# Kernel optimization log

Measured on AMD Instinct MI355X. Metric: run time of the kernel, lower is better.

The kernel has to match this reference:

```python
import jax, jax.numpy as jnp
import numpy as np

C = 2.3026  # Poincare ball curvature
EPS = 1e-15

def _hlinear(x, z, r, c):
    # hypll-style Poincare fully connected layer (HNN++, Shimizu et al.)
    # x: (B, fi) on ball, z: (fi, fo), r: (fo,)
    cs = jnp.sqrt(c)
    lam = 2.0 / (1.0 - c * jnp.sum(x * x, axis=-1, keepdims=True))  # conformal factor (B,1)
    zn = jnp.maximum(jnp.sqrt(jnp.sum(z * z, axis=0)), EPS)         # (fo,)
    tcr = 2.0 * cs * r                                              # (fo,)
    # signed hyperplane distances v_k
    d = (2.0 * zn / cs) * jnp.arcsinh(
        cs * lam * (x @ z) / zn * jnp.cosh(tcr) - (lam - 1.0) * jnp.sinh(tcr))
    w = jnp.sinh(cs * d) / cs
    # map back into the ball: ||out|| < 1/sqrt(c)
    return w / (1.0 + jnp.sqrt(1.0 + c * jnp.sum(w * w, axis=-1, keepdims=True)))

def _hrelu(x, c):
    # logmap at origin -> ReLU in tangent space -> expmap at origin
    cs = jnp.sqrt(c)
    n = jnp.maximum(jnp.sqrt(jnp.sum(x * x, axis=-1, keepdims=True)), EPS)
    v = jnp.arctanh(jnp.minimum(cs * n, 1.0 - 1e-7)) * x / (cs * n)
    v = jax.nn.relu(v)
    vn = jnp.maximum(jnp.sqrt(jnp.sum(v * v, axis=-1, keepdims=True)), EPS)
    return jnp.tanh(cs * vn) * v / (cs * vn)

def setup_inputs() -> dict:
    key = jax.random.key(0)
    ks = jax.random.split(key, 9)
    B, D = 65536, 768
    xs = 0.02 * jax.random.normal(ks[0], (B, D), dtype=jnp.float32)
    # repo preprocessing: lift to Lorentz (K=C) then Lorentz->Poincare
    x0 = jnp.sqrt(1.0 / C + jnp.sum(xs * xs, axis=-1, keepdims=True))
    x = xs / (x0 + 1.0)  # strictly inside ball of radius 1/sqrt(C)
    def mk(k, fi, fo):
        return (jax.random.normal(k, (fi, fo), dtype=jnp.float32) / np.float32(np.sqrt(fi)))
    return {
        "x": x,
        "z1": mk(ks[1], 768, 512), "b1": 0.01 * jax.random.normal(ks[2], (512,), dtype=jnp.float32),
        "z2": mk(ks[3], 512, 256), "b2": 0.01 * jax.random.normal(ks[4], (256,), dtype=jnp.float32),
        "z3": mk(ks[5], 256, 128), "b3": 0.01 * jax.random.normal(ks[6], (128,), dtype=jnp.float32),
        "z4": mk(ks[7], 128, 1),   "b4": 0.01 * jax.random.normal(ks[8], (1,), dtype=jnp.float32),
    }

def reference(x, z1, b1, z2, b2, z3, b3, z4, b4):
    h = _hrelu(_hlinear(x, z1, b1, C), C)
    h = _hrelu(_hlinear(h, z2, b2, C), C)
    h = _hrelu(_hlinear(h, z3, b3, C), C)
    return _hlinear(h, z4, b4, C)
```

## Files before the change

kernel.cpp:

```cpp
#include <hip/hip_runtime.h>

#define CURV 2.3026f
#define EPSF 1e-15f

typedef __attribute__((ext_vector_type(8))) short bfrag8;
typedef __attribute__((ext_vector_type(4))) float ffrag4;

static __device__ __forceinline__ unsigned short f2bf(float f) {
  unsigned u = __builtin_bit_cast(unsigned, f);
  u += 0x7fffu + ((u >> 16) & 1u);
  return (unsigned short)(u >> 16);
}

static __device__ __forceinline__ void gld16(const void* g, void* l) {
  unsigned lo = (unsigned)(unsigned long long)l;
  __builtin_amdgcn_global_load_lds(
      (const __attribute__((address_space(1))) unsigned int*)g,
      (__attribute__((address_space(3))) unsigned int*)lo, 16, 0, 0);
}

__global__ void prep_tiled(const float* __restrict__ z1, const float* __restrict__ r1,
                           const float* __restrict__ z2, const float* __restrict__ r2,
                           const float* __restrict__ z3, const float* __restrict__ r3,
                           const float* __restrict__ z4, const float* __restrict__ r4,
                           unsigned short* __restrict__ zT1, float* __restrict__ st1,
                           unsigned short* __restrict__ zT2, float* __restrict__ st2,
                           unsigned short* __restrict__ zT3, float* __restrict__ st3,
                           unsigned short* __restrict__ zT4, float* __restrict__ st4) {
  int b = blockIdx.x, t = threadIdx.x;
  const float *z, *rv; unsigned short* zT; float* st; int K, N, nt;
  if (b < 8)       { z = z1; rv = r1; zT = zT1; st = st1; K = 768; N = 512; nt = b; }
  else if (b < 12) { z = z2; rv = r2; zT = zT2; st = st2; K = 512; N = 256; nt = b - 8; }
  else if (b < 14) { z = z3; rv = r3; zT = zT3; st = st3; K = 256; N = 128; nt = b - 12; }
  else             { z = z4; rv = r4; zT = zT4; st = st4; K = 128; N = 1;   nt = 0; }
  const float cs = sqrtf(CURV);
  if (N == 1) {
    float v = (t < K) ? z[t] : 0.f;
    if (t < K) zT[t] = f2bf(v);
    float ssl = v * v;
    __shared__ float red4[4];
    for (int m = 1; m <= 32; m <<= 1) ssl += __shfl_xor(ssl, m);
    if ((t & 63) == 0) red4[t >> 6] = ssl;
    __syncthreads();
    if (t == 0) {
      float ss = red4[0] + red4[1] + red4[2] + red4[3];
      float zn = fmaxf(sqrtf(ss), EPSF);
      float tc = 2.f * cs * rv[0];
      st[0] = 2.f * (zn - 1.f); st[1] = coshf(tc) / zn; st[2] = sinhf(tc); st[3] = 0.f;
    }
    return;
  }
  __shared__ unsigned short tile[64 * 72];
  __shared__ float red[4][64];
  const int c = t & 63, rq = t >> 6;
  const int n0 = nt * 64;
  float ssl = 0.f;
  for (int kk = 0; kk < K; kk += 64) {
#pragma unroll
    for (int p = 0; p < 16; p++) {
      int k = kk + 4 * p + rq;
      float v = z[(size_t)k * N + n0 + c];
      ssl += v * v;
      tile[c * 72 + 4 * p + rq] = f2bf(v);
    }
    __syncthreads();
    {
      int wr = t >> 2, seg = t & 3;
      const unsigned long long* src = (const unsigned long long*)(tile + wr * 72 + seg * 16);
      unsigned long long* dst = (unsigned long long*)(zT + (size_t)(n0 + wr) * K + kk + seg * 16);
      dst[0] = src[0]; dst[1] = src[1]; dst[2] = src[2]; dst[3] = src[3];
    }
    __syncthreads();
  }
  red[rq][c] = ssl; __syncthreads();
  if (t < 64) {
    float ss = red[0][t] + red[1][t] + red[2][t] + red[3][t];
    float zn = fmaxf(sqrtf(ss), EPSF);
    float tc = 2.f * cs * rv[n0 + t];
    st[4 * (n0 + t) + 0] = 2.f * (zn - 1.f);
    st[4 * (n0 + t) + 1] = coshf(tc) / zn;
    st[4 * (n0 + t) + 2] = sinhf(tc);
    st[4 * (n0 + t) + 3] = 0.f;
  }
}

template<int NT>
static __device__ __forceinline__ void poly_w(ffrag4 (&acc)[2][NT], const float* __restrict__ stats,
                                              int wn, int lm, int wm, int quad,
                                              const float* lamP, float cs, float inv_cs) {
#pragma unroll
  for (int tn = 0; tn < NT; tn++) {
    float4 st = *(const float4*)(stats + 4 * (wn * (16 * NT) + 16 * tn + lm));
    float dl = st.x, chozn = st.y, sh = st.z;
#pragma unroll
    for (int tm = 0; tm < 2; tm++) {
#pragma unroll
      for (int rg = 0; rg < 4; rg++) {
        float lam = lamP[32 * wm + 16 * tm + 4 * quad + rg];
        float g = cs * lam * acc[tm][tn][rg] * chozn - (lam - 1.f) * sh;
        float q = g * g;
        float u = g * (1.f - q * (1.f / 6.f) + q * q * 0.075f - q * q * q * 0.044642857f);
        float d1 = dl * u;
        float S = 2.f * g * sqrtf(1.f + q);
        float Ch = 1.f + 2.f * q;
        acc[tm][tn][rg] = (S * (1.f + 0.5f * d1 * d1) + Ch * d1) * inv_cs;
      }
    }
  }
}

template<int NT, bool L4>
static __device__ __forceinline__ void reduce_rows(ffrag4 (&acc)[2][NT], const float* z4v,
                                                   int lm, int wm, int quad, float (*sums_)[64]) {
#pragma unroll
  for (int tm = 0; tm < 2; tm++) {
#pragma unroll
    for (int rg = 0; rg < 4; rg++) {
      float s2 = 0.f, sp2 = 0.f, s4 = 0.f;
#pragma unroll
      for (int tn = 0; tn < NT; tn++) {
        float w = acc[tm][tn][rg];
        s2 += w * w;
        float wp = fmaxf(w, 0.f);
        sp2 += wp * wp;
        if (L4) s4 += wp * z4v[tn];
      }
#pragma unroll
      for (int m = 1; m <= 8; m <<= 1) {
        s2 += __shfl_xor(s2, m, 16);
        sp2 += __shfl_xor(sp2, m, 16);
        if (L4) s4 += __shfl_xor(s4, m, 16);
      }
      if (lm == 0) {
        int row = 32 * wm + 16 * tm + 4 * quad + rg;
        atomicAdd(&sums_[0][row], s2);
        atomicAdd(&sums_[1][row], sp2);
        if (L4) atomicAdd(&sums_[2][row], s4);
      }
    }
  }
}

template<int NT>
static __device__ __forceinline__ void panel_write(ffrag4 (&acc)[2][NT], char* panel,
                                                   int lm, int wm, int wn, int quad,
                                                   const float* gamP) {
#pragma unroll
  for (int tm = 0; tm < 2; tm++)
#pragma unroll
    for (int rg = 0; rg < 4; rg++) {
      const int r = 32 * wm + 16 * tm + 4 * quad + rg;
      const float gam = gamP[r];
      const unsigned rb = (unsigned)((r >> 1) * 128);
      const unsigned rx = (unsigned)((r >> 1) & 7);
      const unsigned c0 = (unsigned)((r & 1) * 4);
#pragma unroll
      for (int tn = 0; tn < NT; tn++) {
        const int col = wn * (16 * NT) + 16 * tn + lm;
        const unsigned ad = (unsigned)((col >> 5) * 4096) + rb +
                            (((c0 + (unsigned)((col >> 3) & 3)) ^ rx) << 4) +
                            (unsigned)((col & 7) * 2);
        *(unsigned short*)(panel + ad) = f2bf(gam * fmaxf(acc[tm][tn][rg], 0.f));
      }
    }
}

static __device__ __forceinline__ float stage_a2(float2 f, char* p) {
  unsigned lo = f2bf(f.x), hi = f2bf(f.y);
  *(unsigned*)p = lo | (hi << 16);
  return f.x * f.x + f.y * f.y;
}

__launch_bounds__(1024, 8)
__global__ void fused_mlp(const float* __restrict__ x,
                          const unsigned short* __restrict__ zt1, const float* __restrict__ st1,
                          const unsigned short* __restrict__ zt2, const float* __restrict__ st2,
                          const unsigned short* __restrict__ zt3, const float* __restrict__ st3,
                          const float* __restrict__ z4, const float* __restrict__ st4,
                          float* __restrict__ outF) {
  __shared__ __align__(16) char smem[73728];
  __shared__ float lamS[64];
  __shared__ float gamS[64];
  __shared__ float sums[3][64];

  const int t = threadIdx.x;
  const int wid = t >> 6, lane = t & 63;
  const int wm = wid >> 3, wn = wid & 7;
  const int lm = lane & 15, quad = lane >> 4;
  const int l7 = lane & 7, rl8 = lane >> 3;
  const unsigned rowg0 = blockIdx.x * 64u;

  char* const A1 = smem;
  char* const B1 = smem + 8192;
  char* const H1 = smem;
  char* const H2 = smem;

  const unsigned cB = (unsigned)(l7 ^ rl8);

  const unsigned sl16 = (unsigned)(((((lm & 1) << 2) + quad) ^ (lm >> 1)) << 4);
  unsigned afoff[2];
#pragma unroll
  for (int tm = 0; tm < 2; tm++) afoff[tm] = (unsigned)((16 * wm + 8 * tm + (lm >> 1)) * 128) + sl16;
  unsigned bf1off[4];
#pragma unroll
  for (int tn = 0; tn < 4; tn++) bf1off[tn] = (unsigned)((wn * 32 + 8 * tn + (lm >> 1)) * 128) + sl16;

  const int mrow = 4 * wid + quad;
  const char* a1g = (const char*)x + (size_t)(rowg0 + (unsigned)mrow) * 3072 + (size_t)lm * 8;
  const unsigned a1d = (unsigned)(mrow >> 1) * 128u +
                       ((((unsigned)(mrow & 1) * 4u + ((unsigned)lm >> 2)) ^ ((unsigned)(mrow >> 1) & 7u)) << 4) +
                       ((unsigned)lm & 3u) * 4u;

  unsigned b1s[2], b1d[2];
#pragma unroll
  for (int j = 0; j < 2; j++) {
    unsigned rr = (unsigned)(wid + 16 * j);
    unsigned N_ = 16u * rr + 2u * (unsigned)rl8 + (cB >> 2);
    b1s[j] = N_ * 1536u + (cB & 3u) * 16u;
    b1d[j] = rr * 1024u + (unsigned)lane * 16u;
  }

  float ss = 0.f;
  {
    float2 p0 = *(const float2*)a1g;
    ss += stage_a2(p0, A1 + a1d);
  }
  float2 pA = *(const float2*)(a1g + 128);
  gld16((const char*)zt1 + b1s[0], B1 + b1d[0]);
  gld16((const char*)zt1 + b1s[1], B1 + b1d[1]);

  ffrag4 acc1[2][4];
#pragma unroll
  for (int a = 0; a < 2; a++)
#pragma unroll
    for (int b = 0; b < 4; b++) acc1[a][b] = (ffrag4){0.f, 0.f, 0.f, 0.f};

  for (int k = 0; k < 24; k++) {
    __syncthreads();
    char* curA = A1 + (k & 1) * 4096;
    char* curB = B1 + (k & 1) * 32768;
    if (k < 23) {
      char* nA = A1 + ((k + 1) & 1) * 4096;
      char* nB = B1 + ((k + 1) & 1) * 32768;
      unsigned adv = (unsigned)(k + 1) * 64u;
      gld16((const char*)zt1 + b1s[0] + adv, nB + b1d[0]);
      gld16((const char*)zt1 + b1s[1] + adv, nB + b1d[1]);
      ss += stage_a2(pA, nA + a1d);
      if (k < 22) pA = *(const float2*)(a1g + (size_t)(k + 2) * 128);
    }
    bfrag8 a0 = *(const bfrag8*)(curA + afoff[0]);
    bfrag8 a1f = *(const bfrag8*)(curA + afoff[1]);
#pragma unroll
    for (int tn = 0; tn < 4; tn++) {
      bfrag8 bf = *(const bfrag8*)(curB + bf1off[tn]);
      acc1[0][tn] = __builtin_amdgcn_mfma_f32_16x16x32_bf16(a0, bf, acc1[0][tn], 0, 0, 0);
      acc1[1][tn] = __builtin_amdgcn_mfma_f32_16x16x32_bf16(a1f, bf, acc1[1][tn], 0, 0, 0);
    }
  }

  __syncthreads();

  ss += __shfl_xor(ss, 1); ss += __shfl_xor(ss, 2);
  ss += __shfl_xor(ss, 4); ss += __shfl_xor(ss, 8);
  if (lm == 0) lamS[mrow] = 2.f / (1.f - CURV * ss);
  if (t < 64) { sums[0][t] = 0.f; sums[1][t] = 0.f; }
  __syncthreads();

  const float cs = sqrtf(CURV), inv_cs = 1.f / cs;
  poly_w<4>(acc1, st1, wn, lm, wm, quad, lamS, cs, inv_cs);
  reduce_rows<4, false>(acc1, nullptr, lm, wm, quad, sums);
  __syncthreads();
  if (t < 64) {
    float sw2 = sums[0][t], swp2 = sums[1][t];
    float den = 1.f + sqrtf(1.f + CURV * sw2);
    float nn = fmaxf(sqrtf(sw2) / den, EPSF);
    float al = atanhf(fminf(cs * nn, 1.f - 1e-7f)) / (cs * nn);
    float vn = fmaxf(al * sqrtf(swp2) / den, EPSF);
    float be = tanhf(cs * vn) / (cs * vn);
    float gam = al * be / den;
    gamS[t] = gam;
    lamS[t] = 2.f / (1.f - CURV * gam * gam * swp2);
    sums[0][t] = 0.f; sums[1][t] = 0.f;
  }
  __syncthreads();
  panel_write<4>(acc1, H1, lm, wm, wn, quad, gamS);
  __syncthreads();

  ffrag4 acc2[2][2];
#pragma unroll
  for (int a = 0; a < 2; a++)
#pragma unroll
    for (int b = 0; b < 2; b++) acc2[a][b] = (ffrag4){0.f, 0.f, 0.f, 0.f};

  const char* b2base = (const char*)zt2 + (size_t)(32 * wn + lm) * 1024 + (size_t)quad * 16;
#pragma unroll 4
  for (int kt = 0; kt < 16; kt++) {
    bfrag8 b0 = *(const bfrag8*)(b2base + kt * 64);
    bfrag8 b1v = *(const bfrag8*)(b2base + 16384 + kt * 64);
    bfrag8 a0 = *(const bfrag8*)(H1 + kt * 4096 + afoff[0]);
    bfrag8 a1f = *(const bfrag8*)(H1 + kt * 4096 + afoff[1]);
    acc2[0][0] = __builtin_amdgcn_mfma_f32_16x16x32_bf16(a0,  b0,  acc2[0][0], 0, 0, 0);
    acc2[0][1] = __builtin_amdgcn_mfma_f32_16x16x32_bf16(a0,  b1v, acc2[0][1], 0, 0, 0);
    acc2[1][0] = __builtin_amdgcn_mfma_f32_16x16x32_bf16(a1f, b0,  acc2[1][0], 0, 0, 0);
    acc2[1][1] = __builtin_amdgcn_mfma_f32_16x16x32_bf16(a1f, b1v, acc2[1][1], 0, 0, 0);
  }
  __syncthreads();

  poly_w<2>(acc2, st2, wn, lm, wm, quad, lamS, cs, inv_cs);
  reduce_rows<2, false>(acc2, nullptr, lm, wm, quad, sums);
  __syncthreads();
  if (t < 64) {
    float sw2 = sums[0][t], swp2 = sums[1][t];
    float den = 1.f + sqrtf(1.f + CURV * sw2);
    float nn = fmaxf(sqrtf(sw2) / den, EPSF);
    float al = atanhf(fminf(cs * nn, 1.f - 1e-7f)) / (cs * nn);
    float vn = fmaxf(al * sqrtf(swp2) / den, EPSF);
    float be = tanhf(cs * vn) / (cs * vn);
    float gam = al * be / den;
    gamS[t] = gam;
    lamS[t] = 2.f / (1.f - CURV * gam * gam * swp2);
    sums[0][t] = 0.f; sums[1][t] = 0.f; sums[2][t] = 0.f;
  }
  __syncthreads();
  panel_write<2>(acc2, H2, lm, wm, wn, quad, gamS);
  __syncthreads();

  ffrag4 acc3[2][1];
  acc3[0][0] = (ffrag4){0.f, 0.f, 0.f, 0.f};
  acc3[1][0] = (ffrag4){0.f, 0.f, 0.f, 0.f};
  float z4v[1] = { z4[wn * 16 + lm] };

  const char* b3base = (const char*)zt3 + (size_t)(16 * wn + lm) * 512 + (size_t)quad * 16;
#pragma unroll 4
  for (int kt = 0; kt < 8; kt++) {
    bfrag8 bf = *(const bfrag8*)(b3base + kt * 64);
    bfrag8 a0 = *(const bfrag8*)(H2 + kt * 4096 + afoff[0]);
    bfrag8 a1f = *(const bfrag8*)(H2 + kt * 4096 + afoff[1]);
    acc3[0][0] = __builtin_amdgcn_mfma_f32_16x16x32_bf16(a0,  bf, acc3[0][0], 0, 0, 0);
    acc3[1][0] = __builtin_amdgcn_mfma_f32_16x16x32_bf16(a1f, bf, acc3[1][0], 0, 0, 0);
  }

  poly_w<1>(acc3, st3, wn, lm, wm, quad, lamS, cs, inv_cs);
  reduce_rows<1, true>(acc3, z4v, lm, wm, quad, sums);
  __syncthreads();
  if (t < 64) {
    float sw2 = sums[0][t], swp2 = sums[1][t];
    float den = 1.f + sqrtf(1.f + CURV * sw2);
    float nn = fmaxf(sqrtf(sw2) / den, EPSF);
    float al = atanhf(fminf(cs * nn, 1.f - 1e-7f)) / (cs * nn);
    float vn = fmaxf(al * sqrtf(swp2) / den, EPSF);
    float be = tanhf(cs * vn) / (cs * vn);
    float gam = al * be / den;
    float s = gam * sums[2][t];
    float lamh = 2.f / (1.f - CURV * gam * gam * swp2);
    float g = cs * lamh * s * st4[1] - (lamh - 1.f) * st4[2];
    float q = g * g;
    float u = g * (1.f - q * (1.f / 6.f) + q * q * 0.075f - q * q * q * 0.044642857f);
    float d1 = st4[0] * u;
    float S = 2.f * g * sqrtf(1.f + q);
    float Ch = 1.f + 2.f * q;
    float w = (S * (1.f + 0.5f * d1 * d1) + Ch * d1) * inv_cs;
    outF[rowg0 + t] = w / (1.f + sqrtf(1.f + CURV * w * w));
  }
}

extern "C" void kernel_launch(void* const* d_in, const int* in_sizes, int n_in,
                              void* d_out, int out_size, void* d_ws, size_t ws_size,
                              hipStream_t stream) {
  const float* x  = (const float*)d_in[0];
  const float* z1 = (const float*)d_in[1];
  const float* b1 = (const float*)d_in[2];
  const float* z2 = (const float*)d_in[3];
  const float* b2 = (const float*)d_in[4];
  const float* z3 = (const float*)d_in[5];
  const float* b3 = (const float*)d_in[6];
  const float* z4 = (const float*)d_in[7];
  const float* b4 = (const float*)d_in[8];

  char* ws = (char*)d_ws; size_t off = 0;
  auto carve = [&](size_t b) { char* p = ws + off; off += (b + 255) & ~(size_t)255; return p; };
  unsigned short* zT1 = (unsigned short*)carve(512 * 768 * 2);
  unsigned short* zT2 = (unsigned short*)carve(256 * 512 * 2);
  unsigned short* zT3 = (unsigned short*)carve(128 * 256 * 2);
  unsigned short* zT4 = (unsigned short*)carve(128 * 2);
  float* st1 = (float*)carve(512 * 4 * 4);
  float* st2 = (float*)carve(256 * 4 * 4);
  float* st3 = (float*)carve(128 * 4 * 4);
  float* st4 = (float*)carve(4 * 4);

  prep_tiled<<<15, 256, 0, stream>>>(z1, b1, z2, b2, z3, b3, z4, b4,
                                     zT1, st1, zT2, st2, zT3, st3, zT4, st4);
  fused_mlp<<<1024, 1024, 0, stream>>>(x, zT1, st1, zT2, st2, zT3, st3, z4, st4, (float*)d_out);
}
```

Before: 506.5 us.

## Halve fused MLP block to 8 waves and parallelize weight preprocessing

The fused MLP kernel now runs 512 threads (8 waves) per block instead of 1024. Each wave covers twice as many output columns in every layer, and the activation tile is staged with float4 loads and 4-wide bf16 stores. This is meant to raise per-wave MFMA reuse of the A fragments and to lower barrier cost, at the price of more accumulator registers per thread. Weight preprocessing is split into a 137-block transpose kernel that accumulates column norms atomically, plus a small stats kernel and a memset, replacing the 15-block serial loop.

After: 429.0 us. 15.3% less time.

```diff
diff --git a/kernel.cpp b/kernel.cpp
--- a/kernel.cpp
+++ b/kernel.cpp
@@ -19,69 +19,69 @@
       (__attribute__((address_space(3))) unsigned int*)lo, 16, 0, 0);
 }
 
-__global__ void prep_tiled(const float* __restrict__ z1, const float* __restrict__ r1,
-                           const float* __restrict__ z2, const float* __restrict__ r2,
-                           const float* __restrict__ z3, const float* __restrict__ r3,
-                           const float* __restrict__ z4, const float* __restrict__ r4,
-                           unsigned short* __restrict__ zT1, float* __restrict__ st1,
-                           unsigned short* __restrict__ zT2, float* __restrict__ st2,
-                           unsigned short* __restrict__ zT3, float* __restrict__ st3,
-                           unsigned short* __restrict__ zT4, float* __restrict__ st4) {
+__global__ void prep_transpose(const float* __restrict__ z1, const float* __restrict__ z2,
+                               const float* __restrict__ z3, const float* __restrict__ z4,
+                               unsigned short* __restrict__ zT1, unsigned short* __restrict__ zT2,
+                               unsigned short* __restrict__ zT3, unsigned short* __restrict__ zT4,
+                               float* __restrict__ ssA) {
   int b = blockIdx.x, t = threadIdx.x;
-  const float *z, *rv; unsigned short* zT; float* st; int K, N, nt;
-  if (b < 8)       { z = z1; rv = r1; zT = zT1; st = st1; K = 768; N = 512; nt = b; }
-  else if (b < 12) { z = z2; rv = r2; zT = zT2; st = st2; K = 512; N = 256; nt = b - 8; }
-  else if (b < 14) { z = z3; rv = r3; zT = zT3; st = st3; K = 256; N = 128; nt = b - 12; }
-  else             { z = z4; rv = r4; zT = zT4; st = st4; K = 128; N = 1;   nt = 0; }
-  const float cs = sqrtf(CURV);
-  if (N == 1) {
-    float v = (t < K) ? z[t] : 0.f;
-    if (t < K) zT[t] = f2bf(v);
+  const float* z; unsigned short* zT; int K, N, kt, ct, sbase;
+  if (b < 96)       { z = z1; zT = zT1; K = 768; N = 512; kt = b / 8;  ct = b & 7;        sbase = 0; }
+  else if (b < 128) { int bb = b - 96;  z = z2; zT = zT2; K = 512; N = 256; kt = bb / 4; ct = bb & 3; sbase = 512; }
+  else if (b < 136) { int bb = b - 128; z = z3; zT = zT3; K = 256; N = 128; kt = bb / 2; ct = bb & 1; sbase = 768; }
+  else {
+    float v = (t < 128) ? z4[t] : 0.f;
+    if (t < 128) zT4[t] = f2bf(v);
     float ssl = v * v;
+    for (int m = 1; m <= 32; m <<= 1) ssl += __shfl_xor(ssl, m);
     __shared__ float red4[4];
-    for (int m = 1; m <= 32; m <<= 1) ssl += __shfl_xor(ssl, m);
     if ((t & 63) == 0) red4[t >> 6] = ssl;
     __syncthreads();
-    if (t == 0) {
-      float ss = red4[0] + red4[1] + red4[2] + red4[3];
-      float zn = fmaxf(sqrtf(ss), EPSF);
-      float tc = 2.f * cs * rv[0];
-      st[0] = 2.f * (zn - 1.f); st[1] = coshf(tc) / zn; st[2] = sinhf(tc); st[3] = 0.f;
-    }
+    if (t == 0) atomicAdd(&ssA[896], red4[0] + red4[1] + red4[2] + red4[3]);
     return;
   }
   __shared__ unsigned short tile[64 * 72];
   __shared__ float red[4][64];
   const int c = t & 63, rq = t >> 6;
-  const int n0 = nt * 64;
+  const int n0 = ct * 64, k0 = kt * 64;
   float ssl = 0.f;
-  for (int kk = 0; kk < K; kk += 64) {
-#pragma unroll
-    for (int p = 0; p < 16; p++) {
-      int k = kk + 4 * p + rq;
-      float v = z[(size_t)k * N + n0 + c];
-      ssl += v * v;
-      tile[c * 72 + 4 * p + rq] = f2bf(v);
-    }
-    __syncthreads();
-    {
-      int wr = t >> 2, seg = t & 3;
-      const unsigned long long* src = (const unsigned long long*)(tile + wr * 72 + seg * 16);
-      unsigned long long* dst = (unsigned long long*)(zT + (size_t)(n0 + wr) * K + kk + seg * 16);
-      dst[0] = src[0]; dst[1] = src[1]; dst[2] = src[2]; dst[3] = src[3];
-    }
-    __syncthreads();
-  }
-  red[rq][c] = ssl; __syncthreads();
-  if (t < 64) {
-    float ss = red[0][t] + red[1][t] + red[2][t] + red[3][t];
-    float zn = fmaxf(sqrtf(ss), EPSF);
-    float tc = 2.f * cs * rv[n0 + t];
-    st[4 * (n0 + t) + 0] = 2.f * (zn - 1.f);
-    st[4 * (n0 + t) + 1] = coshf(tc) / zn;
-    st[4 * (n0 + t) + 2] = sinhf(tc);
-    st[4 * (n0 + t) + 3] = 0.f;
-  }
+#pragma unroll
+  for (int p = 0; p < 16; p++) {
+    int k = k0 + 4 * p + rq;
+    float v = z[(size_t)k * N + n0 + c];
+    ssl += v * v;
+    tile[c * 72 + 4 * p + rq] = f2bf(v);
+  }
+  red[rq][c] = ssl;
+  __syncthreads();
+  {
+    int wr = t >> 2, seg = t & 3;
+    const unsigned long long* src = (const unsigned long long*)(tile + wr * 72 + seg * 16);
+    unsigned long long* dst = (unsigned long long*)(zT + (size_t)(n0 + wr) * K + k0 + seg * 16);
+    dst[0] = src[0]; dst[1] = src[1]; dst[2] = src[2]; dst[3] = src[3];
+  }
+  if (t < 64) atomicAdd(&ssA[sbase + n0 + t], red[0][t] + red[1][t] + red[2][t] + red[3][t]);
+}
+
+__global__ void prep_stats(const float* __restrict__ ssA,
+                           const float* __restrict__ r1, const float* __restrict__ r2,
+                           const float* __restrict__ r3, const float* __restrict__ r4,
+                           float* __restrict__ st1, float* __restrict__ st2,
+                           float* __restrict__ st3, float* __restrict__ st4) {
+  int i = blockIdx.x * 512 + threadIdx.x;
+  if (i >= 897) return;
+  const float* rv; float* st; int n;
+  if (i < 512)      { rv = r1; st = st1; n = i; }
+  else if (i < 768) { rv = r2; st = st2; n = i - 512; }
+  else if (i < 896) { rv = r3; st = st3; n = i - 768; }
+  else              { rv = r4; st = st4; n = 0; }
+  float cs = sqrtf(CURV);
+  float zn = fmaxf(sqrtf(ssA[i]), EPSF);
+  float tc = 2.f * cs * rv[n];
+  st[4 * n + 0] = 2.f * (zn - 1.f);
+  st[4 * n + 1] = coshf(tc) / zn;
+  st[4 * n + 2] = sinhf(tc);
+  st[4 * n + 3] = 0.f;
 }
 
 template<int NT>
@@ -165,13 +165,13 @@
     }
 }
 
-static __device__ __forceinline__ float stage_a2(float2 f, char* p) {
-  unsigned lo = f2bf(f.x), hi = f2bf(f.y);
-  *(unsigned*)p = lo | (hi << 16);
-  return f.x * f.x + f.y * f.y;
-}
-
-__launch_bounds__(1024, 8)
+static __device__ __forceinline__ float stage_a4(float4 f, char* p) {
+  ushort4 h; h.x = f2bf(f.x); h.y = f2bf(f.y); h.z = f2bf(f.z); h.w = f2bf(f.w);
+  *(ushort4*)p = h;
+  return f.x * f.x + f.y * f.y + f.z * f.z + f.w * f.w;
+}
+
+__launch_bounds__(512, 4)
 __global__ void fused_mlp(const float* __restrict__ x,
                           const unsigned short* __restrict__ zt1, const float* __restrict__ st1,
                           const unsigned short* __restrict__ zt2, const float* __restrict__ st2,
@@ -185,7 +185,7 @@
 
   const int t = threadIdx.x;
   const int wid = t >> 6, lane = t & 63;
-  const int wm = wid >> 3, wn = wid & 7;
+  const int wm = wid >> 2, wn = wid & 3;
   const int lm = lane & 15, quad = lane >> 4;
   const int l7 = lane & 7, rl8 = lane >> 3;
   const unsigned rowg0 = blockIdx.x * 64u;
@@ -201,20 +201,20 @@
   unsigned afoff[2];
 #pragma unroll
   for (int tm = 0; tm < 2; tm++) afoff[tm] = (unsigned)((16 * wm + 8 * tm + (lm >> 1)) * 128) + sl16;
-  unsigned bf1off[4];
-#pragma unroll
-  for (int tn = 0; tn < 4; tn++) bf1off[tn] = (unsigned)((wn * 32 + 8 * tn + (lm >> 1)) * 128) + sl16;
-
-  const int mrow = 4 * wid + quad;
-  const char* a1g = (const char*)x + (size_t)(rowg0 + (unsigned)mrow) * 3072 + (size_t)lm * 8;
+  unsigned bf1off[8];
+#pragma unroll
+  for (int tn = 0; tn < 8; tn++) bf1off[tn] = (unsigned)((wn * 64 + 8 * tn + (lm >> 1)) * 128) + sl16;
+
+  const int mrow = 8 * wid + rl8;
+  const char* a1g = (const char*)x + (size_t)(rowg0 + (unsigned)mrow) * 3072 + (size_t)l7 * 16;
   const unsigned a1d = (unsigned)(mrow >> 1) * 128u +
-                       ((((unsigned)(mrow & 1) * 4u + ((unsigned)lm >> 2)) ^ ((unsigned)(mrow >> 1) & 7u)) << 4) +
-                       ((unsigned)lm & 3u) * 4u;
-
-  unsigned b1s[2], b1d[2];
-#pragma unroll
-  for (int j = 0; j < 2; j++) {
-    unsigned rr = (unsigned)(wid + 16 * j);
+                       ((((unsigned)(mrow & 1) * 4u + ((unsigned)l7 >> 1)) ^ ((unsigned)(mrow >> 1) & 7u)) << 4) +
+                       ((unsigned)l7 & 1u) * 8u;
+
+  unsigned b1s[4], b1d[4];
+#pragma unroll
+  for (int j = 0; j < 4; j++) {
+    unsigned rr = (unsigned)(wid + 8 * j);
     unsigned N_ = 16u * rr + 2u * (unsigned)rl8 + (cB >> 2);
     b1s[j] = N_ * 1536u + (cB & 3u) * 16u;
     b1d[j] = rr * 1024u + (unsigned)lane * 16u;
@@ -222,18 +222,18 @@
 
   float ss = 0.f;
   {
-    float2 p0 = *(const float2*)a1g;
-    ss += stage_a2(p0, A1 + a1d);
-  }
-  float2 pA = *(const float2*)(a1g + 128);
-  gld16((const char*)zt1 + b1s[0], B1 + b1d[0]);
-  gld16((const char*)zt1 + b1s[1], B1 + b1d[1]);
-
-  ffrag4 acc1[2][4];
+    float4 p0 = *(const float4*)a1g;
+    ss += stage_a4(p0, A1 + a1d);
+  }
+  float4 pA = *(const float4*)(a1g + 128);
+#pragma unroll
+  for (int j = 0; j < 4; j++) gld16((const char*)zt1 + b1s[j], B1 + b1d[j]);
+
+  ffrag4 acc1[2][8];
 #pragma unroll
   for (int a = 0; a < 2; a++)
 #pragma unroll
-    for (int b = 0; b < 4; b++) acc1[a][b] = (ffrag4){0.f, 0.f, 0.f, 0.f};
+    for (int b = 0; b < 8; b++) acc1[a][b] = (ffrag4){0.f, 0.f, 0.f, 0.f};
 
   for (int k = 0; k < 24; k++) {
     __syncthreads();
@@ -243,15 +243,15 @@
       char* nA = A1 + ((k + 1) & 1) * 4096;
       char* nB = B1 + ((k + 1) & 1) * 32768;
       unsigned adv = (unsigned)(k + 1) * 64u;
-      gld16((const char*)zt1 + b1s[0] + adv, nB + b1d[0]);
-      gld16((const char*)zt1 + b1s[1] + adv, nB + b1d[1]);
-      ss += stage_a2(pA, nA + a1d);
-      if (k < 22) pA = *(const float2*)(a1g + (size_t)(k + 2) * 128);
+#pragma unroll
+      for (int j = 0; j < 4; j++) gld16((const char*)zt1 + b1s[j] + adv, nB + b1d[j]);
+      ss += stage_a4(pA, nA + a1d);
+      if (k < 22) pA = *(const float4*)(a1g + (size_t)(k + 2) * 128);
     }
     bfrag8 a0 = *(const bfrag8*)(curA + afoff[0]);
     bfrag8 a1f = *(const bfrag8*)(curA + afoff[1]);
 #pragma unroll
-    for (int tn = 0; tn < 4; tn++) {
+    for (int tn = 0; tn < 8; tn++) {
       bfrag8 bf = *(const bfrag8*)(curB + bf1off[tn]);
       acc1[0][tn] = __builtin_amdgcn_mfma_f32_16x16x32_bf16(a0, bf, acc1[0][tn], 0, 0, 0);
       acc1[1][tn] = __builtin_amdgcn_mfma_f32_16x16x32_bf16(a1f, bf, acc1[1][tn], 0, 0, 0);
@@ -260,15 +260,14 @@
 
   __syncthreads();
 
-  ss += __shfl_xor(ss, 1); ss += __shfl_xor(ss, 2);
-  ss += __shfl_xor(ss, 4); ss += __shfl_xor(ss, 8);
-  if (lm == 0) lamS[mrow] = 2.f / (1.f - CURV * ss);
+  ss += __shfl_xor(ss, 1); ss += __shfl_xor(ss, 2); ss += __shfl_xor(ss, 4);
+  if (l7 == 0) lamS[mrow] = 2.f / (1.f - CURV * ss);
   if (t < 64) { sums[0][t] = 0.f; sums[1][t] = 0.f; }
   __syncthreads();
 
   const float cs = sqrtf(CURV), inv_cs = 1.f / cs;
-  poly_w<4>(acc1, st1, wn, lm, wm, quad, lamS, cs, inv_cs);
-  reduce_rows<4, false>(acc1, nullptr, lm, wm, quad, sums);
+  poly_w<8>(acc1, st1, wn, lm, wm, quad, lamS, cs, inv_cs);
+  reduce_rows<8, false>(acc1, nullptr, lm, wm, quad, sums);
   __syncthreads();
   if (t < 64) {
     float sw2 = sums[0][t], swp2 = sums[1][t];
@@ -283,31 +282,31 @@
     sums[0][t] = 0.f; sums[1][t] = 0.f;
   }
   __syncthreads();
-  panel_write<4>(acc1, H1, lm, wm, wn, quad, gamS);
-  __syncthreads();
-
-  ffrag4 acc2[2][2];
+  panel_write<8>(acc1, H1, lm, wm, wn, quad, gamS);
+  __syncthreads();
+
+  ffrag4 acc2[2][4];
 #pragma unroll
   for (int a = 0; a < 2; a++)
 #pragma unroll
-    for (int b = 0; b < 2; b++) acc2[a][b] = (ffrag4){0.f, 0.f, 0.f, 0.f};
-
-  const char* b2base = (const char*)zt2 + (size_t)(32 * wn + lm) * 1024 + (size_t)quad * 16;
+    for (int b = 0; b < 4; b++) acc2[a][b] = (ffrag4){0.f, 0.f, 0.f, 0.f};
+
+  const char* b2base = (const char*)zt2 + (size_t)(64 * wn + lm) * 1024 + (size_t)quad * 16;
 #pragma unroll 4
   for (int kt = 0; kt < 16; kt++) {
-    bfrag8 b0 = *(const bfrag8*)(b2base + kt * 64);
-    bfrag8 b1v = *(const bfrag8*)(b2base + 16384 + kt * 64);
     bfrag8 a0 = *(const bfrag8*)(H1 + kt * 4096 + afoff[0]);
     bfrag8 a1f = *(const bfrag8*)(H1 + kt * 4096 + afoff[1]);
-    acc2[0][0] = __builtin_amdgcn_mfma_f32_16x16x32_bf16(a0,  b0,  acc2[0][0], 0, 0, 0);
-    acc2[0][1] = __builtin_amdgcn_mfma_f32_16x16x32_bf16(a0,  b1v, acc2[0][1], 0, 0, 0);
-    acc2[1][0] = __builtin_amdgcn_mfma_f32_16x16x32_bf16(a1f, b0,  acc2[1][0], 0, 0, 0);
-    acc2[1][1] = __builtin_amdgcn_mfma_f32_16x16x32_bf16(a1f, b1v, acc2[1][1], 0, 0, 0);
-  }
-  __syncthreads();
-
-  poly_w<2>(acc2, st2, wn, lm, wm, quad, lamS, cs, inv_cs);
-  reduce_rows<2, false>(acc2, nullptr, lm, wm, quad, sums);
+#pragma unroll
+    for (int tn = 0; tn < 4; tn++) {
+      bfrag8 bv = *(const bfrag8*)(b2base + (size_t)tn * 16384 + kt * 64);
+      acc2[0][tn] = __builtin_amdgcn_mfma_f32_16x16x32_bf16(a0,  bv, acc2[0][tn], 0, 0, 0);
+      acc2[1][tn] = __builtin_amdgcn_mfma_f32_16x16x32_bf16(a1f, bv, acc2[1][tn], 0, 0, 0);
+    }
+  }
+  __syncthreads();
+
+  poly_w<4>(acc2, st2, wn, lm, wm, quad, lamS, cs, inv_cs);
+  reduce_rows<4, false>(acc2, nullptr, lm, wm, quad, sums);
   __syncthreads();
   if (t < 64) {
     float sw2 = sums[0][t], swp2 = sums[1][t];
@@ -322,26 +321,31 @@
     sums[0][t] = 0.f; sums[1][t] = 0.f; sums[2][t] = 0.f;
   }
   __syncthreads();
-  panel_write<2>(acc2, H2, lm, wm, wn, quad, gamS);
-  __syncthreads();
-
-  ffrag4 acc3[2][1];
-  acc3[0][0] = (ffrag4){0.f, 0.f, 0.f, 0.f};
-  acc3[1][0] = (ffrag4){0.f, 0.f, 0.f, 0.f};
-  float z4v[1] = { z4[wn * 16 + lm] };
-
-  const char* b3base = (const char*)zt3 + (size_t)(16 * wn + lm) * 512 + (size_t)quad * 16;
+  panel_write<4>(acc2, H2, lm, wm, wn, quad, gamS);
+  __syncthreads();
+
+  ffrag4 acc3[2][2];
+#pragma unroll
+  for (int a = 0; a < 2; a++)
+#pragma unroll
+    for (int b = 0; b < 2; b++) acc3[a][b] = (ffrag4){0.f, 0.f, 0.f, 0.f};
+  float z4v[2] = { z4[32 * wn + lm], z4[32 * wn + 16 + lm] };
+
+  const char* b3base = (const char*)zt3 + (size_t)(32 * wn + lm) * 512 + (size_t)quad * 16;
 #pragma unroll 4
   for (int kt = 0; kt < 8; kt++) {
-    bfrag8 bf = *(const bfrag8*)(b3base + kt * 64);
     bfrag8 a0 = *(const bfrag8*)(H2 + kt * 4096 + afoff[0]);
     bfrag8 a1f = *(const bfrag8*)(H2 + kt * 4096 + afoff[1]);
-    acc3[0][0] = __builtin_amdgcn_mfma_f32_16x16x32_bf16(a0,  bf, acc3[0][0], 0, 0, 0);
-    acc3[1][0] = __builtin_amdgcn_mfma_f32_16x16x32_bf16(a1f, bf, acc3[1][0], 0, 0, 0);
-  }
-
-  poly_w<1>(acc3, st3, wn, lm, wm, quad, lamS, cs, inv_cs);
-  reduce_rows<1, true>(acc3, z4v, lm, wm, quad, sums);
+#pragma unroll
+    for (int tn = 0; tn < 2; tn++) {
+      bfrag8 bv = *(const bfrag8*)(b3base + (size_t)tn * 8192 + kt * 64);
+      acc3[0][tn] = __builtin_amdgcn_mfma_f32_16x16x32_bf16(a0,  bv, acc3[0][tn], 0, 0, 0);
+      acc3[1][tn] = __builtin_amdgcn_mfma_f32_16x16x32_bf16(a1f, bv, acc3[1][tn], 0, 0, 0);
+    }
+  }
+
+  poly_w<2>(acc3, st3, wn, lm, wm, quad, lamS, cs, inv_cs);
+  reduce_rows<2, true>(acc3, z4v, lm, wm, quad, sums);
   __syncthreads();
   if (t < 64) {
     float sw2 = sums[0][t], swp2 = sums[1][t];
@@ -387,8 +391,10 @@
   float* st2 = (float*)carve(256 * 4 * 4);
   float* st3 = (float*)carve(128 * 4 * 4);
   float* st4 = (float*)carve(4 * 4);
-
-  prep_tiled<<<15, 256, 0, stream>>>(z1, b1, z2, b2, z3, b3, z4, b4,
-                                     zT1, st1, zT2, st2, zT3, st3, zT4, st4);
-  fused_mlp<<<1024, 1024, 0, stream>>>(x, zT1, st1, zT2, st2, zT3, st3, z4, st4, (float*)d_out);
-}
+  float* ssA = (float*)carve(897 * 4);
+
+  hipMemsetAsync(ssA, 0, 897 * 4, stream);
+  prep_transpose<<<137, 256, 0, stream>>>(z1, z2, z3, z4, zT1, zT2, zT3, zT4, ssA);
+  prep_stats<<<2, 512, 0, stream>>>(ssA, b1, b2, b3, b4, st1, st2, st3, st4);
+  fused_mlp<<<1024, 512, 0, stream>>>(x, zT1, st1, zT2, st2, zT3, st3, z4, st4, (float*)d_out);
+}
```
